# Kernel tuning notes

Hardware: AMD Instinct MI355X
Metric: run time of the kernel (lower is better)

Reference implementation:

```python
import jax, jax.numpy as jnp
import numpy as np

SEQ, B, CIN, H, K = 2048, 16, 512, 512, 2

def setup_inputs() -> dict:
    key = jax.random.key(0)
    k1, k2, k3 = jax.random.split(key, 3)
    x = jax.random.normal(k1, (SEQ, B, CIN), dtype=jnp.float32)
    W = jax.random.normal(k2, (3 * H, CIN, K), dtype=jnp.float32) * (1.0 / np.sqrt(CIN * K))
    b = jax.random.normal(k3, (3 * H,), dtype=jnp.float32) * 0.01
    return {"x": x, "W": W, "b": b}

def _qrnn_fo(x, W, b):
    # x: (T, B, Cin) -> conv input (B, Cin, T), causal left pad of K-1 zeros
    xb = jnp.transpose(x, (1, 2, 0))
    g = jax.lax.conv_general_dilated(
        xb, W, window_strides=(1,), padding=[(K - 1, 0)],
        dimension_numbers=("NCH", "OIH", "NCH"))
    g = g + b[None, :, None]
    g = jnp.transpose(g, (2, 0, 1))  # (T, B, 3H)
    zg, fg, og = jnp.split(g, 3, axis=-1)
    z = jnp.tanh(zg)
    f = jax.nn.sigmoid(fg)
    o = jax.nn.sigmoid(og)

    def step(c, gates_t):
        zt, ft, ot = gates_t
        c = ft * c + (1.0 - ft) * zt
        h = c * ot
        return c, h

    c0 = jnp.zeros((B, H), dtype=x.dtype)
    c_last, hs = jax.lax.scan(step, c0, (z, f, o))
    return hs, c_last

def reference(x, W, b):
    hs, c_last = _qrnn_fo(x, W, b)
    h_last = hs[-1]
    return hs, h_last[None, :], c_last[None, :]
```

## Files before the change

### kernel.cpp

```cpp
#include <hip/hip_runtime.h>

#define SEQ   2048
#define BATCH 16
#define CINCH 512
#define HDIM  512
#define NDIM  1536
#define TBM   (SEQ*BATCH)
#define KRED  1024
#define NCH   64
#define CHL   32
#define NCOL  8192

typedef unsigned short ushort_t;
typedef __bf16 bf16x8 __attribute__((ext_vector_type(8)));
typedef unsigned short u16x8 __attribute__((ext_vector_type(8)));
typedef float f32x4 __attribute__((ext_vector_type(4)));

__device__ __forceinline__ float bf2f(ushort_t u) {
    return __uint_as_float(((unsigned int)u) << 16);
}
__device__ __forceinline__ ushort_t f2bf(float x) {
    unsigned int u = __float_as_uint(x);
    unsigned int r = u + 0x7fffu + ((u >> 16) & 1u);
    return (ushort_t)(r >> 16);
}

__global__ void cast_x_kernel(const float* __restrict__ x, ushort_t* __restrict__ xb) {
    int i = blockIdx.x * 256 + threadIdx.x;
    int e = i * 4;
    ushort4 r;
    if (e < BATCH * CINCH) {
        r.x = 0; r.y = 0; r.z = 0; r.w = 0;
    } else {
        float4 v = *(const float4*)(x + (e - BATCH * CINCH));
        r.x = f2bf(v.x); r.y = f2bf(v.y); r.z = f2bf(v.z); r.w = f2bf(v.w);
    }
    *(ushort4*)(xb + e) = r;
}

__global__ void repack_w_kernel(const float* __restrict__ W, ushort_t* __restrict__ wb) {
    int i = blockIdx.x * 256 + threadIdx.x;
    int o  = i >> 10;
    int r  = i & 1023;
    int k  = r >> 9;
    int ci = r & 511;
    wb[i] = f2bf(W[o * 1024 + ci * 2 + k]);
}

__device__ __forceinline__ void load_lds_16B(const ushort_t* g, ushort_t* l) {
    auto* gp = reinterpret_cast<const __attribute__((address_space(1))) unsigned int*>(
        reinterpret_cast<uintptr_t>(g));
    auto* lp = reinterpret_cast<__attribute__((address_space(3))) unsigned int*>(
        reinterpret_cast<uintptr_t>(l));
    __builtin_amdgcn_global_load_lds(gp, lp, 16, 0, 0);
}

__global__ __launch_bounds__(256) void gemm_gates_kernel(
    const ushort_t* __restrict__ xb, const ushort_t* __restrict__ wb,
    const float* __restrict__ bias,
    ushort_t* __restrict__ zb, ushort_t* __restrict__ fb, ushort_t* __restrict__ ob) {

    __shared__ ushort_t smem[2 * 128 * 64];
    ushort_t* As = smem;
    ushort_t* Bs = smem + 128 * 64;

    const int tid  = threadIdx.x;
    const int w    = tid >> 6;
    const int lane = tid & 63;
    const int quad = lane >> 4;
    const int l15  = lane & 15;
    const int wm   = w & 1;
    const int wn   = w >> 1;
    const int mBase = blockIdx.x * 128;
    const int nBase = blockIdx.y * 128;

    const int srow = lane >> 3;
    const int scb  = lane & 7;

    f32x4 acc[4][4];
#pragma unroll
    for (int i = 0; i < 4; ++i)
#pragma unroll
        for (int j = 0; j < 4; ++j)
            acc[i][j] = (f32x4){0.f, 0.f, 0.f, 0.f};

    for (int kt = 0; kt < 16; ++kt) {
        __syncthreads();
        const long aOff = (kt < 8) ? (long)kt * 64 : (long)16 * 512 + (long)(kt - 8) * 64;
#pragma unroll
        for (int i = 0; i < 4; ++i) {
            const int row = w * 32 + i * 8 + srow;
            const int cbd = scb ^ (row & 7);
            const ushort_t* ga = xb + (long)(mBase + row) * 512 + aOff + cbd * 8;
            load_lds_16B(ga, &As[(w * 32 + i * 8) * 64]);
            const ushort_t* gb = wb + (long)(nBase + row) * 1024 + kt * 64 + cbd * 8;
            load_lds_16B(gb, &Bs[(w * 32 + i * 8) * 64]);
        }
        __syncthreads();

#pragma unroll
        for (int ks = 0; ks < 2; ++ks) {
            bf16x8 af[4], bfr[4];
            const int cbd = ks * 4 + quad;
#pragma unroll
            for (int mt = 0; mt < 4; ++mt) {
                int ml  = wm * 64 + mt * 16 + l15;
                int off = ml * 64 + ((cbd ^ (ml & 7)) * 8);
                af[mt] = __builtin_bit_cast(bf16x8, *(const u16x8*)(&As[off]));
            }
#pragma unroll
            for (int nt = 0; nt < 4; ++nt) {
                int nl  = wn * 64 + nt * 16 + l15;
                int off = nl * 64 + ((cbd ^ (nl & 7)) * 8);
                bfr[nt] = __builtin_bit_cast(bf16x8, *(const u16x8*)(&Bs[off]));
            }
#pragma unroll
            for (int mt = 0; mt < 4; ++mt)
#pragma unroll
                for (int nt = 0; nt < 4; ++nt)
                    acc[mt][nt] = __builtin_amdgcn_mfma_f32_16x16x32_bf16(
                        af[mt], bfr[nt], acc[mt][nt], 0, 0, 0);
        }
    }

    const int gate = nBase >> 9;
    const int hb   = nBase & 511;

    __syncthreads();
#pragma unroll
    for (int nt = 0; nt < 4; ++nt) {
        const int n_local = wn * 64 + nt * 16 + l15;
        const float bv = bias[nBase + n_local];
#pragma unroll
        for (int mt = 0; mt < 4; ++mt) {
#pragma unroll
            for (int r = 0; r < 4; ++r) {
                const int m_local = wm * 64 + mt * 16 + quad * 4 + r;
                float g = acc[mt][nt][r] + bv;
                float a;
                if (gate == 0) {
                    float e = __expf(-2.f * fabsf(g));
                    float t = (1.f - e) / (1.f + e);
                    a = copysignf(t, g);
                } else {
                    a = 1.f / (1.f + __expf(-g));
                }
                const int phys = ((n_local >> 3) ^ (m_local & 7)) * 8 + (n_local & 7);
                smem[m_local * 128 + phys] = f2bf(a);
            }
        }
    }
    __syncthreads();

    ushort_t* outp = (gate == 0) ? zb : (gate == 1) ? fb : ob;
#pragma unroll
    for (int s = 0; s < 8; ++s) {
        const int m_local = w * 32 + s * 4 + quad;
        const int blk = l15 ^ (m_local & 7);
        u16x8 v = *(const u16x8*)(&smem[m_local * 128 + blk * 8]);
        *(u16x8*)(outp + (long)(mBase + m_local) * 512 + hb + l15 * 8) = v;
    }
}

__device__ __forceinline__ void scan_step(float z, float f, float& A, float& Bv) {
    Bv = f * Bv + (1.f - f) * z;
    A *= f;
}

__global__ __launch_bounds__(256) void scan_compose(
    const ushort_t* __restrict__ zb, const ushort_t* __restrict__ fb,
    float* __restrict__ Acomp, float* __restrict__ Bcomp) {
    const int cg  = (blockIdx.x & 7) * 256 + threadIdx.x;
    const int ch  = blockIdx.x >> 3;
    const int col = cg * 4;
    const long base = (long)ch * CHL * NCOL + col;
    float Ax = 1.f, Ay = 1.f, Az = 1.f, Aw = 1.f;
    float Bx = 0.f, By = 0.f, Bz = 0.f, Bw = 0.f;
    const int U = 8;
    for (int w0 = 0; w0 < CHL; w0 += U) {
        ushort4 zr[U], fr[U];
#pragma unroll
        for (int u = 0; u < U; ++u) {
            const long idx = base + (long)(w0 + u) * NCOL;
            zr[u] = *(const ushort4*)(zb + idx);
            fr[u] = *(const ushort4*)(fb + idx);
        }
#pragma unroll
        for (int u = 0; u < U; ++u) {
            scan_step(bf2f(zr[u].x), bf2f(fr[u].x), Ax, Bx);
            scan_step(bf2f(zr[u].y), bf2f(fr[u].y), Ay, By);
            scan_step(bf2f(zr[u].z), bf2f(fr[u].z), Az, Bz);
            scan_step(bf2f(zr[u].w), bf2f(fr[u].w), Aw, Bw);
        }
    }
    *(float4*)(Acomp + (long)ch * NCOL + col) = make_float4(Ax, Ay, Az, Aw);
    *(float4*)(Bcomp + (long)ch * NCOL + col) = make_float4(Bx, By, Bz, Bw);
}

__global__ void scan_prefix(const float* __restrict__ Acomp,
                            const float* __restrict__ Bcomp,
                            float* __restrict__ Cin) {
    const int col = blockIdx.x * 256 + threadIdx.x;
    float c = 0.f;
#pragma unroll 4
    for (int ch = 0; ch < NCH; ++ch) {
        Cin[ch * NCOL + col] = c;
        c = Acomp[ch * NCOL + col] * c + Bcomp[ch * NCOL + col];
    }
}

__global__ __launch_bounds__(256) void scan_apply(
    const ushort_t* __restrict__ zb, const ushort_t* __restrict__ fb,
    const ushort_t* __restrict__ ob, const float* __restrict__ Cin,
    float* __restrict__ out) {
    const int cg  = (blockIdx.x & 7) * 256 + threadIdx.x;
    const int ch  = blockIdx.x >> 3;
    const int col = cg * 4;
    const long base = (long)ch * CHL * NCOL + col;
    float4 c0 = *(const float4*)(Cin + (long)ch * NCOL + col);
    float cx = c0.x, cy = c0.y, cz = c0.z, cw = c0.w;
    float hx = 0.f, hy = 0.f, hz = 0.f, hw = 0.f;
    const int U = 8;
    for (int w0 = 0; w0 < CHL; w0 += U) {
        ushort4 zr[U], fr[U], orr[U];
#pragma unroll
        for (int u = 0; u < U; ++u) {
            const long idx = base + (long)(w0 + u) * NCOL;
            zr[u]  = *(const ushort4*)(zb + idx);
            fr[u]  = *(const ushort4*)(fb + idx);
            orr[u] = *(const ushort4*)(ob + idx);
        }
#pragma unroll
        for (int u = 0; u < U; ++u) {
            float f, z;
            f = bf2f(fr[u].x); z = bf2f(zr[u].x); cx = f * cx + (1.f - f) * z; hx = cx * bf2f(orr[u].x);
            f = bf2f(fr[u].y); z = bf2f(zr[u].y); cy = f * cy + (1.f - f) * z; hy = cy * bf2f(orr[u].y);
            f = bf2f(fr[u].z); z = bf2f(zr[u].z); cz = f * cz + (1.f - f) * z; hz = cz * bf2f(orr[u].z);
            f = bf2f(fr[u].w); z = bf2f(zr[u].w); cw = f * cw + (1.f - f) * z; hw = cw * bf2f(orr[u].w);
            *(float4*)(out + base + (long)(w0 + u) * NCOL) = make_float4(hx, hy, hz, hw);
        }
    }
    if (ch == NCH - 1) {
        *(float4*)(out + (long)SEQ * NCOL + col)        = make_float4(hx, hy, hz, hw);
        *(float4*)(out + (long)SEQ * NCOL + NCOL + col) = make_float4(cx, cy, cz, cw);
    }
}

extern "C" void kernel_launch(void* const* d_in, const int* in_sizes, int n_in,
                              void* d_out, int out_size, void* d_ws, size_t ws_size,
                              hipStream_t stream) {
    const float* x  = (const float*)d_in[0];
    const float* W  = (const float*)d_in[1];
    const float* bi = (const float*)d_in[2];
    float* out = (float*)d_out;

    char* ws = (char*)d_ws;
    const size_t xbN = (size_t)(TBM + BATCH) * CINCH;
    const size_t wbN = (size_t)NDIM * KRED;
    const size_t gN  = (size_t)TBM * HDIM;
    ushort_t* xb = (ushort_t*)ws;
    ushort_t* wb = (ushort_t*)(ws + xbN * 2);
    ushort_t* zb = (ushort_t*)(ws + xbN * 2 + wbN * 2);
    ushort_t* fb = zb + gN;
    ushort_t* ob = fb + gN;
    float* Acomp = (float*)ws;
    float* Bcomp = Acomp + NCH * NCOL;
    float* Cin   = Bcomp + NCH * NCOL;

    cast_x_kernel<<<16392, 256, 0, stream>>>(x, xb);
    repack_w_kernel<<<6144, 256, 0, stream>>>(W, wb);
    dim3 ggrid(TBM / 128, NDIM / 128);
    gemm_gates_kernel<<<ggrid, 256, 0, stream>>>(xb, wb, bi, zb, fb, ob);
    scan_compose<<<NCH * 8, 256, 0, stream>>>(zb, fb, Acomp, Bcomp);
    scan_prefix<<<NCOL / 256, 256, 0, stream>>>(Acomp, Bcomp, Cin);
    scan_apply<<<NCH * 8, 256, 0, stream>>>(zb, fb, ob, Cin, out);
}
```

Baseline: 298.6 us.

## Fuse prep kernels, drop scan_prefix by recomputing carry in apply, use nontemporal IO

After: 274.2 us. 1.09x faster.

```diff
diff --git a/kernel.cpp b/kernel.cpp
--- a/kernel.cpp
+++ b/kernel.cpp
@@ -7,13 +7,14 @@
 #define NDIM  1536
 #define TBM   (SEQ*BATCH)
 #define KRED  1024
-#define NCH   64
-#define CHL   32
+#define NCH   32
+#define CHL   64
 #define NCOL  8192
 
 typedef unsigned short ushort_t;
 typedef __bf16 bf16x8 __attribute__((ext_vector_type(8)));
 typedef unsigned short u16x8 __attribute__((ext_vector_type(8)));
+typedef unsigned short u16x4 __attribute__((ext_vector_type(4)));
 typedef float f32x4 __attribute__((ext_vector_type(4)));
 
 __device__ __forceinline__ float bf2f(ushort_t u) {
@@ -25,26 +26,28 @@
     return (ushort_t)(r >> 16);
 }
 
-__global__ void cast_x_kernel(const float* __restrict__ x, ushort_t* __restrict__ xb) {
-    int i = blockIdx.x * 256 + threadIdx.x;
-    int e = i * 4;
-    ushort4 r;
-    if (e < BATCH * CINCH) {
-        r.x = 0; r.y = 0; r.z = 0; r.w = 0;
+#define CAST_BLOCKS 16392
+__global__ void prep_kernel(const float* __restrict__ x, ushort_t* __restrict__ xb,
+                            const float* __restrict__ W, ushort_t* __restrict__ wb) {
+    if (blockIdx.x < CAST_BLOCKS) {
+        int i = blockIdx.x * 256 + threadIdx.x;
+        int e = i * 4;
+        ushort4 r;
+        if (e < BATCH * CINCH) {
+            r.x = 0; r.y = 0; r.z = 0; r.w = 0;
+        } else {
+            float4 v = *(const float4*)(x + (e - BATCH * CINCH));
+            r.x = f2bf(v.x); r.y = f2bf(v.y); r.z = f2bf(v.z); r.w = f2bf(v.w);
+        }
+        *(ushort4*)(xb + e) = r;
     } else {
-        float4 v = *(const float4*)(x + (e - BATCH * CINCH));
-        r.x = f2bf(v.x); r.y = f2bf(v.y); r.z = f2bf(v.z); r.w = f2bf(v.w);
-    }
-    *(ushort4*)(xb + e) = r;
-}
-
-__global__ void repack_w_kernel(const float* __restrict__ W, ushort_t* __restrict__ wb) {
-    int i = blockIdx.x * 256 + threadIdx.x;
-    int o  = i >> 10;
-    int r  = i & 1023;
-    int k  = r >> 9;
-    int ci = r & 511;
-    wb[i] = f2bf(W[o * 1024 + ci * 2 + k]);
+        int i = (blockIdx.x - CAST_BLOCKS) * 256 + threadIdx.x;
+        int o  = i >> 10;
+        int r  = i & 1023;
+        int k  = r >> 9;
+        int ci = r & 511;
+        wb[i] = f2bf(W[o * 1024 + ci * 2 + k]);
+    }
 }
 
 __device__ __forceinline__ void load_lds_16B(const ushort_t* g, ushort_t* l) {
@@ -167,6 +170,10 @@
     A *= f;
 }
 
+__device__ __forceinline__ u16x4 ntload_u4(const ushort_t* p) {
+    return __builtin_nontemporal_load((const u16x4*)p);
+}
+
 __global__ __launch_bounds__(256) void scan_compose(
     const ushort_t* __restrict__ zb, const ushort_t* __restrict__ fb,
     float* __restrict__ Acomp, float* __restrict__ Bcomp) {
@@ -178,71 +185,70 @@
     float Bx = 0.f, By = 0.f, Bz = 0.f, Bw = 0.f;
     const int U = 8;
     for (int w0 = 0; w0 < CHL; w0 += U) {
-        ushort4 zr[U], fr[U];
+        u16x4 zr[U], fr[U];
 #pragma unroll
         for (int u = 0; u < U; ++u) {
             const long idx = base + (long)(w0 + u) * NCOL;
-            zr[u] = *(const ushort4*)(zb + idx);
-            fr[u] = *(const ushort4*)(fb + idx);
-        }
-#pragma unroll
-        for (int u = 0; u < U; ++u) {
-            scan_step(bf2f(zr[u].x), bf2f(fr[u].x), Ax, Bx);
-            scan_step(bf2f(zr[u].y), bf2f(fr[u].y), Ay, By);
-            scan_step(bf2f(zr[u].z), bf2f(fr[u].z), Az, Bz);
-            scan_step(bf2f(zr[u].w), bf2f(fr[u].w), Aw, Bw);
-        }
-    }
-    *(float4*)(Acomp + (long)ch * NCOL + col) = make_float4(Ax, Ay, Az, Aw);
-    *(float4*)(Bcomp + (long)ch * NCOL + col) = make_float4(Bx, By, Bz, Bw);
-}
-
-__global__ void scan_prefix(const float* __restrict__ Acomp,
-                            const float* __restrict__ Bcomp,
-                            float* __restrict__ Cin) {
-    const int col = blockIdx.x * 256 + threadIdx.x;
-    float c = 0.f;
-#pragma unroll 4
-    for (int ch = 0; ch < NCH; ++ch) {
-        Cin[ch * NCOL + col] = c;
-        c = Acomp[ch * NCOL + col] * c + Bcomp[ch * NCOL + col];
-    }
+            zr[u] = *(const u16x4*)(zb + idx);
+            fr[u] = *(const u16x4*)(fb + idx);
+        }
+#pragma unroll
+        for (int u = 0; u < U; ++u) {
+            scan_step(bf2f(zr[u][0]), bf2f(fr[u][0]), Ax, Bx);
+            scan_step(bf2f(zr[u][1]), bf2f(fr[u][1]), Ay, By);
+            scan_step(bf2f(zr[u][2]), bf2f(fr[u][2]), Az, Bz);
+            scan_step(bf2f(zr[u][3]), bf2f(fr[u][3]), Aw, Bw);
+        }
+    }
+    *(f32x4*)(Acomp + (long)ch * NCOL + col) = (f32x4){Ax, Ay, Az, Aw};
+    *(f32x4*)(Bcomp + (long)ch * NCOL + col) = (f32x4){Bx, By, Bz, Bw};
 }
 
 __global__ __launch_bounds__(256) void scan_apply(
     const ushort_t* __restrict__ zb, const ushort_t* __restrict__ fb,
-    const ushort_t* __restrict__ ob, const float* __restrict__ Cin,
+    const ushort_t* __restrict__ ob,
+    const float* __restrict__ Acomp, const float* __restrict__ Bcomp,
     float* __restrict__ out) {
     const int cg  = (blockIdx.x & 7) * 256 + threadIdx.x;
     const int ch  = blockIdx.x >> 3;
     const int col = cg * 4;
     const long base = (long)ch * CHL * NCOL + col;
-    float4 c0 = *(const float4*)(Cin + (long)ch * NCOL + col);
-    float cx = c0.x, cy = c0.y, cz = c0.z, cw = c0.w;
+
+    float cx = 0.f, cy = 0.f, cz = 0.f, cw = 0.f;
+    for (int k = 0; k < ch; ++k) {
+        f32x4 a4 = *(const f32x4*)(Acomp + (long)k * NCOL + col);
+        f32x4 b4 = *(const f32x4*)(Bcomp + (long)k * NCOL + col);
+        cx = a4[0] * cx + b4[0];
+        cy = a4[1] * cy + b4[1];
+        cz = a4[2] * cz + b4[2];
+        cw = a4[3] * cw + b4[3];
+    }
+
     float hx = 0.f, hy = 0.f, hz = 0.f, hw = 0.f;
     const int U = 8;
     for (int w0 = 0; w0 < CHL; w0 += U) {
-        ushort4 zr[U], fr[U], orr[U];
+        u16x4 zr[U], fr[U], orr[U];
 #pragma unroll
         for (int u = 0; u < U; ++u) {
             const long idx = base + (long)(w0 + u) * NCOL;
-            zr[u]  = *(const ushort4*)(zb + idx);
-            fr[u]  = *(const ushort4*)(fb + idx);
-            orr[u] = *(const ushort4*)(ob + idx);
+            zr[u]  = ntload_u4(zb + idx);
+            fr[u]  = ntload_u4(fb + idx);
+            orr[u] = ntload_u4(ob + idx);
         }
 #pragma unroll
         for (int u = 0; u < U; ++u) {
             float f, z;
-            f = bf2f(fr[u].x); z = bf2f(zr[u].x); cx = f * cx + (1.f - f) * z; hx = cx * bf2f(orr[u].x);
-            f = bf2f(fr[u].y); z = bf2f(zr[u].y); cy = f * cy + (1.f - f) * z; hy = cy * bf2f(orr[u].y);
-            f = bf2f(fr[u].z); z = bf2f(zr[u].z); cz = f * cz + (1.f - f) * z; hz = cz * bf2f(orr[u].z);
-            f = bf2f(fr[u].w); z = bf2f(zr[u].w); cw = f * cw + (1.f - f) * z; hw = cw * bf2f(orr[u].w);
-            *(float4*)(out + base + (long)(w0 + u) * NCOL) = make_float4(hx, hy, hz, hw);
+            f = bf2f(fr[u][0]); z = bf2f(zr[u][0]); cx = f * cx + (1.f - f) * z; hx = cx * bf2f(orr[u][0]);
+            f = bf2f(fr[u][1]); z = bf2f(zr[u][1]); cy = f * cy + (1.f - f) * z; hy = cy * bf2f(orr[u][1]);
+            f = bf2f(fr[u][2]); z = bf2f(zr[u][2]); cz = f * cz + (1.f - f) * z; hz = cz * bf2f(orr[u][2]);
+            f = bf2f(fr[u][3]); z = bf2f(zr[u][3]); cw = f * cw + (1.f - f) * z; hw = cw * bf2f(orr[u][3]);
+            f32x4 hv = (f32x4){hx, hy, hz, hw};
+            __builtin_nontemporal_store(hv, (f32x4*)(out + base + (long)(w0 + u) * NCOL));
         }
     }
     if (ch == NCH - 1) {
-        *(float4*)(out + (long)SEQ * NCOL + col)        = make_float4(hx, hy, hz, hw);
-        *(float4*)(out + (long)SEQ * NCOL + NCOL + col) = make_float4(cx, cy, cz, cw);
+        *(f32x4*)(out + (long)SEQ * NCOL + col)        = (f32x4){hx, hy, hz, hw};
+        *(f32x4*)(out + (long)SEQ * NCOL + NCOL + col) = (f32x4){cx, cy, cz, cw};
     }
 }
 
@@ -265,13 +271,10 @@
     ushort_t* ob = fb + gN;
     float* Acomp = (float*)ws;
     float* Bcomp = Acomp + NCH * NCOL;
-    float* Cin   = Bcomp + NCH * NCOL;
-
-    cast_x_kernel<<<16392, 256, 0, stream>>>(x, xb);
-    repack_w_kernel<<<6144, 256, 0, stream>>>(W, wb);
+
+    prep_kernel<<<CAST_BLOCKS + 6144, 256, 0, stream>>>(x, xb, W, wb);
     dim3 ggrid(TBM / 128, NDIM / 128);
     gemm_gates_kernel<<<ggrid, 256, 0, stream>>>(xb, wb, bi, zb, fb, ob);
     scan_compose<<<NCH * 8, 256, 0, stream>>>(zb, fb, Acomp, Bcomp);
-    scan_prefix<<<NCOL / 256, 256, 0, stream>>>(Acomp, Bcomp, Cin);
-    scan_apply<<<NCH * 8, 256, 0, stream>>>(zb, fb, ob, Cin, out);
-}
+    scan_apply<<<NCH * 8, 256, 0, stream>>>(zb, fb, ob, Acomp, Bcomp, out);
+}
```
